# Kernel tuning notes

Measured on AMD Instinct MI355X. Metric: run time of the kernel, lower is better.

The kernel has to match this reference:

```python
import jax, jax.numpy as jnp
import numpy as np

B, NN, T, H, P = 4, 50000, 1, 64, 5   # batch, nodes/graph, time steps, hidden, prediction steps
E = 1_200_000                          # edges over the flattened batched graph
N = B * NN                             # total flattened nodes


def setup_inputs() -> dict:
    key = jax.random.key(0)
    ks = jax.random.split(key, 10)
    x = jax.random.normal(ks[0], (B, NN, T), jnp.float32)
    edge_index = jax.random.randint(ks[1], (2, E), 0, N)
    edge_weight = jax.random.uniform(ks[2], (E,), jnp.float32)
    h = jnp.zeros((B, NN, H), jnp.float32)
    s = lambda k, shp, fan: (jax.random.normal(k, shp, jnp.float32) / np.float32(np.sqrt(fan)))
    W1 = s(ks[3], (T, H), T); b1 = jnp.zeros((H,), jnp.float32)
    W2 = s(ks[4], (H, H), H); b2 = jnp.zeros((H,), jnp.float32)
    w_ih = s(ks[5], (3 * H, H), H)
    w_hh = s(ks[6], (3 * H, H), H)
    b_ih = jnp.zeros((3 * H,), jnp.float32)
    b_hh = jnp.zeros((3 * H,), jnp.float32)
    fc_w = s(ks[7], (H, P), H); fc_b = jnp.zeros((P,), jnp.float32)
    return dict(x=x, edge_weight=edge_weight, h=h, W1=W1, b1=b1, W2=W2, b2=b2,
                w_ih=w_ih, w_hh=w_hh, b_ih=b_ih, b_hh=b_hh, fc_w=fc_w, fc_b=fc_b,
                edge_index=edge_index)


def _gcn(xf, src, dst, ew, dinv, W, b):
    # PyG GCNConv: x' = D^-1/2 (A + I) D^-1/2 (x W) + b, self-loop weight 1
    xw = xf @ W                                  # [N, H]
    norm = dinv[src] * ew * dinv[dst]            # [E]
    agg = jax.ops.segment_sum(xw[src] * norm[:, None], dst, num_segments=N)
    return agg + (dinv * dinv)[:, None] * xw + b  # self-loop term + bias


def reference(x, edge_weight, h, W1, b1, W2, b2, w_ih, w_hh, b_ih, b_hh, fc_w, fc_b, edge_index):
    src, dst = edge_index[0], edge_index[1]
    # degree includes self-loop weight 1 (PyG add_self_loops fill_value=1)
    deg = jax.ops.segment_sum(edge_weight, dst, num_segments=N) + 1.0
    dinv = jax.lax.rsqrt(deg)

    xf = x.reshape(N, T)
    xf = jax.nn.relu(_gcn(xf, src, dst, edge_weight, dinv, W1, b1))
    xf = jax.nn.relu(_gcn(xf, src, dst, edge_weight, dinv, W2, b2))

    # torch GRUCell
    hf = h.reshape(N, H)
    gi = xf @ w_ih.T + b_ih
    gh = hf @ w_hh.T + b_hh
    i_r, i_z, i_n = jnp.split(gi, 3, axis=1)
    h_r, h_z, h_n = jnp.split(gh, 3, axis=1)
    r = jax.nn.sigmoid(i_r + h_r)
    z = jax.nn.sigmoid(i_z + h_z)
    n = jnp.tanh(i_n + r * h_n)
    h_new = (1.0 - z) * n + z * hf

    out = h_new @ fc_w + fc_b
    return out.reshape(B, NN, P), h_new.reshape(B, NN, H)
```

## Files before the change

### kernel.cpp

```cpp
#include <hip/hip_runtime.h>

#define NTOT 200000
#define EE   1200000

typedef unsigned int u32;
typedef unsigned long long u64;
typedef __attribute__((ext_vector_type(8))) short short8v;
typedef __attribute__((ext_vector_type(4))) float f32x4;

__device__ __forceinline__ float rcpf(float x) { return __builtin_amdgcn_rcpf(x); }
__device__ __forceinline__ float sigm(float x) { return rcpf(1.f + __expf(-x)); }
__device__ __forceinline__ float tanh_f(float x) { return 1.f - 2.f * rcpf(__expf(2.f * x) + 1.f); }
__device__ __forceinline__ u32 f2bf(float f) {
    u32 u = __float_as_uint(f);
    return (u + 0x7fffu + ((u >> 16) & 1u)) >> 16;
}
__device__ __forceinline__ float bf2f(u32 b) { return __uint_as_float(b << 16); }
__device__ __forceinline__ float bf_lo(u32 p) { return __uint_as_float(p << 16); }
__device__ __forceinline__ float bf_hi(u32 p) { return __uint_as_float(p & 0xffff0000u); }

__device__ __forceinline__ short8v packhi8(const float* v) {
    union { u32 u[4]; short8v s; } r;
    r.u[0] = f2bf(v[0]) | (f2bf(v[1]) << 16);
    r.u[1] = f2bf(v[2]) | (f2bf(v[3]) << 16);
    r.u[2] = f2bf(v[4]) | (f2bf(v[5]) << 16);
    r.u[3] = f2bf(v[6]) | (f2bf(v[7]) << 16);
    return r.s;
}
__device__ __forceinline__ short8v packlo8(const float* v) {
    float q[8];
    #pragma unroll
    for (int i = 0; i < 8; ++i) q[i] = v[i] - bf2f(f2bf(v[i]));
    union { u32 u[4]; short8v s; } r;
    r.u[0] = f2bf(q[0]) | (f2bf(q[1]) << 16);
    r.u[1] = f2bf(q[2]) | (f2bf(q[3]) << 16);
    r.u[2] = f2bf(q[4]) | (f2bf(q[5]) << 16);
    r.u[3] = f2bf(q[6]) | (f2bf(q[7]) << 16);
    return r.s;
}

__global__ __launch_bounds__(256) void k_degcnt(const float* __restrict__ ew,
                                                const int* __restrict__ dst,
                                                u64* __restrict__ pk,
                                                u32* __restrict__ rank) {
    int e = blockIdx.x*256 + threadIdx.x;
    if (e < EE) {
        u64 v = (1ull << 40) | (u64)(u32)__float2uint_rn(ew[e] * 16777216.f);
        u64 old = atomicAdd(&pk[dst[e]], v);
        rank[e] = (u32)(old >> 40);
    }
}

__global__ __launch_bounds__(256) void k_scan1(const u64* __restrict__ pk,
                                               int* __restrict__ off,
                                               int* __restrict__ bsum,
                                               float* __restrict__ dinv) {
    __shared__ int s[256];
    int t = threadIdx.x, i = blockIdx.x*256 + t;
    int v = 0;
    if (i < NTOT) {
        u64 p = pk[i];
        v = (int)(p >> 40);
        dinv[i] = rsqrtf(1.0f + (float)(p & 0xFFFFFFFFFFull) * 5.9604644775390625e-8f);
    }
    s[t] = v; __syncthreads();
    #pragma unroll
    for (int o = 1; o < 256; o <<= 1) {
        int a = (t >= o) ? s[t-o] : 0; __syncthreads();
        s[t] += a; __syncthreads();
    }
    if (i < NTOT) off[i] = s[t] - v;
    if (t == 255) bsum[blockIdx.x] = s[255];
}

__global__ __launch_bounds__(1024) void k_scan2(int* bsum) {
    __shared__ int s[1024];
    int t = threadIdx.x;
    int v = (t < 782) ? bsum[t] : 0;
    s[t] = v; __syncthreads();
    for (int o = 1; o < 1024; o <<= 1) {
        int a = (t >= o) ? s[t-o] : 0; __syncthreads();
        s[t] += a; __syncthreads();
    }
    if (t < 782) bsum[t] = s[t] - v;
}

__global__ __launch_bounds__(256) void k_scan3(int* __restrict__ off,
                                               const int* __restrict__ bsum) {
    int i = blockIdx.x*256 + threadIdx.x;
    if (i < NTOT) off[i] = off[i] + bsum[blockIdx.x];
    if (i == 0) off[NTOT] = EE;
}

__global__ __launch_bounds__(256) void k_fill(const int* __restrict__ src,
                                              const int* __restrict__ dst,
                                              const float* __restrict__ ew,
                                              const float* __restrict__ dinv,
                                              const int* __restrict__ off,
                                              const u32* __restrict__ rank,
                                              uint2* __restrict__ epack) {
    int e = blockIdx.x*256 + threadIdx.x;
    if (e >= EE) return;
    int d = dst[e], s = src[e];
    float norm = dinv[s] * ew[e] * dinv[d];
    int p = off[d] + (int)rank[e];
    epack[p] = make_uint2((u32)s, __float_as_uint(norm));
}

__global__ __launch_bounds__(256) void k_sagg(const int* __restrict__ off,
                                              const uint2* __restrict__ epack,
                                              const float* __restrict__ x,
                                              const float* __restrict__ dinv,
                                              float* __restrict__ sagg) {
    int n = blockIdx.x*256 + threadIdx.x;
    if (n >= NTOT) return;
    int e0 = off[n], e1 = off[n+1];
    float s = 0.f;
    for (int e = e0; e < e1; ++e) {
        uint2 ep = epack[e];
        s += __uint_as_float(ep.y) * x[ep.x];
    }
    float di = dinv[n];
    sagg[n] = s + di*di*x[n];
}

__global__ __launch_bounds__(256) void k_wprep(const float* __restrict__ wih,
                                               const float* __restrict__ whh,
                                               uint4* __restrict__ wpack) {
    int v = blockIdx.x*256 + threadIdx.x;
    if (v >= 3072) return;
    int lane = v & 63, tau = v >> 6;
    const float* W = (tau < 24) ? wih : whh;
    int tt = tau % 24;
    int lt = tt >> 1, ks = tt & 1;
    const float* s = W + (lt*16 + (lane & 15))*64 + ks*32 + (lane >> 4)*8;
    uint4 o;
    o.x = f2bf(s[0]) | (f2bf(s[1]) << 16);
    o.y = f2bf(s[2]) | (f2bf(s[3]) << 16);
    o.z = f2bf(s[4]) | (f2bf(s[5]) << 16);
    o.w = f2bf(s[6]) | (f2bf(s[7]) << 16);
    wpack[v] = o;
}

__global__ __launch_bounds__(256) void k_l12(const float* __restrict__ sagg,
                                             const float* __restrict__ W1,
                                             const float* __restrict__ b1,
                                             const float* __restrict__ W2,
                                             u32* __restrict__ A2p) {
    __shared__ float ysh[64][68];
    __shared__ float wsh[64*68];
    int t = threadIdx.x;
    int n0 = blockIdx.x * 64;
    #pragma unroll
    for (int i = 0; i < 16; ++i) {
        int v = t + i*256;
        wsh[(v >> 6)*68 + (v & 63)] = W2[v];
    }
    {
        int row = t >> 2, c0 = (t & 3) * 16;
        float sv = sagg[n0 + row];
        #pragma unroll
        for (int q = 0; q < 4; ++q) {
            float4 w  = *(const float4*)(W1 + c0 + q*4);
            float4 bb = *(const float4*)(b1 + c0 + q*4);
            ysh[row][c0+q*4+0] = fmaxf(sv*w.x + bb.x, 0.f);
            ysh[row][c0+q*4+1] = fmaxf(sv*w.y + bb.y, 0.f);
            ysh[row][c0+q*4+2] = fmaxf(sv*w.z + bb.z, 0.f);
            ysh[row][c0+q*4+3] = fmaxf(sv*w.w + bb.w, 0.f);
        }
    }
    __syncthreads();
    int p = t >> 3, c = t & 7;
    float acc0[8], acc1[8];
    #pragma unroll
    for (int j = 0; j < 8; ++j) { acc0[j] = 0.f; acc1[j] = 0.f; }
    #pragma unroll 4
    for (int k = 0; k < 64; ++k) {
        float y0 = ysh[p][k], y1 = ysh[p+32][k];
        const float* wr = wsh + k*68 + c*8;
        float4 w0 = *(const float4*)wr;
        float4 w1 = *(const float4*)(wr + 4);
        acc0[0] += y0*w0.x; acc0[1] += y0*w0.y; acc0[2] += y0*w0.z; acc0[3] += y0*w0.w;
        acc0[4] += y0*w1.x; acc0[5] += y0*w1.y; acc0[6] += y0*w1.z; acc0[7] += y0*w1.w;
        acc1[0] += y1*w0.x; acc1[1] += y1*w0.y; acc1[2] += y1*w0.z; acc1[3] += y1*w0.w;
        acc1[4] += y1*w1.x; acc1[5] += y1*w1.y; acc1[6] += y1*w1.z; acc1[7] += y1*w1.w;
    }
    int na = n0 + p, nb = n0 + p + 32;
    uint4 pk;
    pk.x = f2bf(acc0[0]) | (f2bf(acc0[1]) << 16);
    pk.y = f2bf(acc0[2]) | (f2bf(acc0[3]) << 16);
    pk.z = f2bf(acc0[4]) | (f2bf(acc0[5]) << 16);
    pk.w = f2bf(acc0[6]) | (f2bf(acc0[7]) << 16);
    *(uint4*)(A2p + (size_t)na*32 + c*4) = pk;
    pk.x = f2bf(acc1[0]) | (f2bf(acc1[1]) << 16);
    pk.y = f2bf(acc1[2]) | (f2bf(acc1[3]) << 16);
    pk.z = f2bf(acc1[4]) | (f2bf(acc1[5]) << 16);
    pk.w = f2bf(acc1[6]) | (f2bf(acc1[7]) << 16);
    *(uint4*)(A2p + (size_t)nb*32 + c*4) = pk;
}

__global__ __launch_bounds__(256) void k_gather(const u32* __restrict__ A2p,
                                                const uint2* __restrict__ epack,
                                                const int* __restrict__ off,
                                                const float* __restrict__ dinv,
                                                const float* __restrict__ b2,
                                                float* __restrict__ B2) {
    int wv = (blockIdx.x*256 + threadIdx.x) >> 6;
    int lane = threadIdx.x & 63;
    if (wv >= NTOT) return;
    int g = lane >> 4, q = lane & 15;
    int e0 = off[wv], e1 = off[wv+1];
    float ax = 0.f, ay = 0.f, az = 0.f, aw = 0.f;
    for (int e = e0 + g; e < e1; e += 4) {
        uint2 ep = epack[e];
        int sr = (int)ep.x;
        float nrm = __uint_as_float(ep.y);
        uint2 pw = *(const uint2*)(A2p + (size_t)sr*32 + q*2);
        ax += nrm*bf_lo(pw.x); ay += nrm*bf_hi(pw.x);
        az += nrm*bf_lo(pw.y); aw += nrm*bf_hi(pw.y);
    }
    ax += __shfl_xor(ax, 16); ax += __shfl_xor(ax, 32);
    ay += __shfl_xor(ay, 16); ay += __shfl_xor(ay, 32);
    az += __shfl_xor(az, 16); az += __shfl_xor(az, 32);
    aw += __shfl_xor(aw, 16); aw += __shfl_xor(aw, 32);
    if (g == 0) {
        float di = dinv[wv], d2 = di*di;
        uint2 pw = *(const uint2*)(A2p + (size_t)wv*32 + q*2);
        float4 bb = *(const float4*)(b2 + q*4);
        float4 o;
        o.x = fmaxf(ax + d2*bf_lo(pw.x) + bb.x, 0.f);
        o.y = fmaxf(ay + d2*bf_hi(pw.x) + bb.y, 0.f);
        o.z = fmaxf(az + d2*bf_lo(pw.y) + bb.z, 0.f);
        o.w = fmaxf(aw + d2*bf_hi(pw.y) + bb.w, 0.f);
        *(float4*)(B2 + (size_t)wv*64 + q*4) = o;
    }
}

__global__ __launch_bounds__(256) void k_gru(const float* B2,
                                             const float* __restrict__ h_in,
                                             const uint4* __restrict__ wpack,
                                             const float* __restrict__ bih,
                                             const float* __restrict__ bhh,
                                             const float* __restrict__ fcw,
                                             const float* __restrict__ fcb,
                                             float* __restrict__ out,
                                             float* hnew) {
    int t = threadIdx.x;
    int lane = t & 63, w = t >> 6;
    int n0 = blockIdx.x * 64;
    int rowA = n0 + w*16 + (lane & 15);
    int kb = (lane >> 4) * 8;
    float yf[16], hb[16];
    {
        const float4* yp = (const float4*)(B2 + (size_t)rowA*64 + kb);
        const float4* hp = (const float4*)(h_in + (size_t)rowA*64 + kb);
        *(float4*)&yf[0]  = yp[0]; *(float4*)&yf[4]  = yp[1];
        *(float4*)&yf[8]  = yp[8]; *(float4*)&yf[12] = yp[9];
        *(float4*)&hb[0]  = hp[0]; *(float4*)&hb[4]  = hp[1];
        *(float4*)&hb[8]  = hp[8]; *(float4*)&hb[12] = hp[9];
    }
    short8v ya0h = packhi8(&yf[0]), ya1h = packhi8(&yf[8]);
    short8v ya0l = packlo8(&yf[0]), ya1l = packlo8(&yf[8]);
    short8v ha0h = packhi8(&hb[0]), ha1h = packhi8(&hb[8]);
    short8v ha0l = packlo8(&hb[0]), ha1l = packlo8(&hb[8]);
    float po[4][5] = {};
    #pragma unroll
    for (int lt = 0; lt < 4; ++lt) {
        short8v wbr0 = *(const short8v*)&wpack[(lt*2+0)*64 + lane];
        short8v wbr1 = *(const short8v*)&wpack[(lt*2+1)*64 + lane];
        short8v wbz0 = *(const short8v*)&wpack[((lt+4)*2+0)*64 + lane];
        short8v wbz1 = *(const short8v*)&wpack[((lt+4)*2+1)*64 + lane];
        short8v wbn0 = *(const short8v*)&wpack[((lt+8)*2+0)*64 + lane];
        short8v wbn1 = *(const short8v*)&wpack[((lt+8)*2+1)*64 + lane];
        short8v vbr0 = *(const short8v*)&wpack[1536 + (lt*2+0)*64 + lane];
        short8v vbr1 = *(const short8v*)&wpack[1536 + (lt*2+1)*64 + lane];
        short8v vbz0 = *(const short8v*)&wpack[1536 + ((lt+4)*2+0)*64 + lane];
        short8v vbz1 = *(const short8v*)&wpack[1536 + ((lt+4)*2+1)*64 + lane];
        short8v vbn0 = *(const short8v*)&wpack[1536 + ((lt+8)*2+0)*64 + lane];
        short8v vbn1 = *(const short8v*)&wpack[1536 + ((lt+8)*2+1)*64 + lane];
        f32x4 aR  = {0.f,0.f,0.f,0.f};
        f32x4 aZ  = {0.f,0.f,0.f,0.f};
        f32x4 aNi = {0.f,0.f,0.f,0.f};
        f32x4 aNh = {0.f,0.f,0.f,0.f};
        aR = __builtin_amdgcn_mfma_f32_16x16x32_bf16(ya0h, wbr0, aR, 0, 0, 0);
        aR = __builtin_amdgcn_mfma_f32_16x16x32_bf16(ya1h, wbr1, aR, 0, 0, 0);
        aR = __builtin_amdgcn_mfma_f32_16x16x32_bf16(ya0l, wbr0, aR, 0, 0, 0);
        aR = __builtin_amdgcn_mfma_f32_16x16x32_bf16(ya1l, wbr1, aR, 0, 0, 0);
        aR = __builtin_amdgcn_mfma_f32_16x16x32_bf16(ha0h, vbr0, aR, 0, 0, 0);
        aR = __builtin_amdgcn_mfma_f32_16x16x32_bf16(ha1h, vbr1, aR, 0, 0, 0);
        aR = __builtin_amdgcn_mfma_f32_16x16x32_bf16(ha0l, vbr0, aR, 0, 0, 0);
        aR = __builtin_amdgcn_mfma_f32_16x16x32_bf16(ha1l, vbr1, aR, 0, 0, 0);
        aZ = __builtin_amdgcn_mfma_f32_16x16x32_bf16(ya0h, wbz0, aZ, 0, 0, 0);
        aZ = __builtin_amdgcn_mfma_f32_16x16x32_bf16(ya1h, wbz1, aZ, 0, 0, 0);
        aZ = __builtin_amdgcn_mfma_f32_16x16x32_bf16(ya0l, wbz0, aZ, 0, 0, 0);
        aZ = __builtin_amdgcn_mfma_f32_16x16x32_bf16(ya1l, wbz1, aZ, 0, 0, 0);
        aZ = __builtin_amdgcn_mfma_f32_16x16x32_bf16(ha0h, vbz0, aZ, 0, 0, 0);
        aZ = __builtin_amdgcn_mfma_f32_16x16x32_bf16(ha1h, vbz1, aZ, 0, 0, 0);
        aZ = __builtin_amdgcn_mfma_f32_16x16x32_bf16(ha0l, vbz0, aZ, 0, 0, 0);
        aZ = __builtin_amdgcn_mfma_f32_16x16x32_bf16(ha1l, vbz1, aZ, 0, 0, 0);
        aNi = __builtin_amdgcn_mfma_f32_16x16x32_bf16(ya0h, wbn0, aNi, 0, 0, 0);
        aNi = __builtin_amdgcn_mfma_f32_16x16x32_bf16(ya1h, wbn1, aNi, 0, 0, 0);
        aNi = __builtin_amdgcn_mfma_f32_16x16x32_bf16(ya0l, wbn0, aNi, 0, 0, 0);
        aNi = __builtin_amdgcn_mfma_f32_16x16x32_bf16(ya1l, wbn1, aNi, 0, 0, 0);
        aNh = __builtin_amdgcn_mfma_f32_16x16x32_bf16(ha0h, vbn0, aNh, 0, 0, 0);
        aNh = __builtin_amdgcn_mfma_f32_16x16x32_bf16(ha1h, vbn1, aNh, 0, 0, 0);
        aNh = __builtin_amdgcn_mfma_f32_16x16x32_bf16(ha0l, vbn0, aNh, 0, 0, 0);
        aNh = __builtin_amdgcn_mfma_f32_16x16x32_bf16(ha1l, vbn1, aNh, 0, 0, 0);
        int l = lt*16 + (lane & 15);
        float br = bih[l] + bhh[l];
        float bz = bih[64+l] + bhh[64+l];
        float bn = bih[128+l];
        float cn = bhh[128+l];
        float fw0 = fcw[l*5+0], fw1 = fcw[l*5+1], fw2 = fcw[l*5+2],
              fw3 = fcw[l*5+3], fw4 = fcw[l*5+4];
        #pragma unroll
        for (int r4 = 0; r4 < 4; ++r4) {
            int row = n0 + w*16 + (lane >> 4)*4 + r4;
            float rg = sigm(aR[r4] + br);
            float zg = sigm(aZ[r4] + bz);
            float ng = tanh_f(aNi[r4] + bn + rg*(aNh[r4] + cn));
            float hfv = h_in[(size_t)row*64 + l];
            float hnv = (1.f - zg)*ng + zg*hfv;
            hnew[(size_t)row*64 + l] = hnv;
            po[r4][0] += hnv*fw0; po[r4][1] += hnv*fw1; po[r4][2] += hnv*fw2;
            po[r4][3] += hnv*fw3; po[r4][4] += hnv*fw4;
        }
    }
    #pragma unroll
    for (int r4 = 0; r4 < 4; ++r4)
        #pragma unroll
        for (int j = 0; j < 5; ++j) {
            float v = po[r4][j];
            v += __shfl_xor(v, 1); v += __shfl_xor(v, 2);
            v += __shfl_xor(v, 4); v += __shfl_xor(v, 8);
            po[r4][j] = v;
        }
    if ((lane & 15) == 0) {
        #pragma unroll
        for (int r4 = 0; r4 < 4; ++r4) {
            int node = n0 + w*16 + (lane >> 4)*4 + r4;
            #pragma unroll
            for (int j = 0; j < 5; ++j) out[(size_t)node*5 + j] = po[r4][j] + fcb[j];
        }
    }
}

extern "C" void kernel_launch(void* const* d_in, const int* in_sizes, int n_in,
                              void* d_out, int out_size, void* d_ws, size_t ws_size,
                              hipStream_t stream) {
    const float* x   = (const float*)d_in[0];
    const float* ew  = (const float*)d_in[1];
    const float* h   = (const float*)d_in[2];
    const float* W1  = (const float*)d_in[3];
    const float* b1  = (const float*)d_in[4];
    const float* W2  = (const float*)d_in[5];
    const float* b2  = (const float*)d_in[6];
    const float* wih = (const float*)d_in[7];
    const float* whh = (const float*)d_in[8];
    const float* bih = (const float*)d_in[9];
    const float* bhh = (const float*)d_in[10];
    const float* fcw = (const float*)d_in[11];
    const float* fcb = (const float*)d_in[12];
    const int*   ei  = (const int*)d_in[13];
    const int* src = ei;
    const int* dst = ei + EE;

    u32*   A2p   = (u32*)d_ws;
    uint2* epack = (uint2*)((char*)d_ws + 25600000);
    uint4* wpack = (uint4*)((char*)d_ws + 35200000);
    u64*   pk    = (u64*)((char*)d_ws + 36000000);
    u32*   rank  = (u32*)((char*)d_ws + 38000000);
    int*   off  = (int*)d_out;
    int*   bsum = off + NTOT + 1;
    float* dinv = (float*)d_out + 401024;
    float* sagg = (float*)d_out + 601024;
    float* out  = (float*)d_out;
    float* B2   = out + (size_t)NTOT*5;

    hipMemsetAsync(pk, 0, (size_t)NTOT*8, stream);
    k_degcnt<<<4688,  256, 0, stream>>>(ew, dst, pk, rank);
    k_scan1 <<<782,   256, 0, stream>>>(pk, off, bsum, dinv);
    k_scan2 <<<1,    1024, 0, stream>>>(bsum);
    k_scan3 <<<782,   256, 0, stream>>>(off, bsum);
    k_fill  <<<4688,  256, 0, stream>>>(src, dst, ew, dinv, off, rank, epack);
    k_sagg  <<<782,   256, 0, stream>>>(off, epack, x, dinv, sagg);
    k_wprep <<<12,    256, 0, stream>>>(wih, whh, wpack);
    k_l12   <<<3125,  256, 0, stream>>>(sagg, W1, b1, W2, A2p);
    k_gather<<<50000, 256, 0, stream>>>(A2p, epack, off, dinv, b2, B2);
    k_gru   <<<3125,  256, 0, stream>>>(B2, h, wpack, bih, bhh, fcw, fcb, out, B2);
}
```

Baseline: 279.5 us.

## Fuse layer-2 edge gather into GRU kernel via shared-memory staging

Merges the per-node gather kernel (second GCN aggregation) into the GRU/MFMA kernel. Each wave gathers 16 nodes sequentially into shared memory, and h is staged in shared memory too, so the fp32 B2 intermediate never goes to and from global memory and one launch is removed. In exchange, each wave walks its 16 nodes serially, which cuts memory-level parallelism for the latency-bound gather. Scratch arrays are also moved from the output buffer into the workspace.

```diff
diff --git a/kernel.cpp b/kernel.cpp
--- a/kernel.cpp
+++ b/kernel.cpp
@@ -199,66 +199,70 @@
     *(uint4*)(A2p + (size_t)nb*32 + c*4) = pk;
 }
 
-__global__ __launch_bounds__(256) void k_gather(const u32* __restrict__ A2p,
-                                                const uint2* __restrict__ epack,
-                                                const int* __restrict__ off,
-                                                const float* __restrict__ dinv,
-                                                const float* __restrict__ b2,
-                                                float* __restrict__ B2) {
-    int wv = (blockIdx.x*256 + threadIdx.x) >> 6;
-    int lane = threadIdx.x & 63;
-    if (wv >= NTOT) return;
-    int g = lane >> 4, q = lane & 15;
-    int e0 = off[wv], e1 = off[wv+1];
-    float ax = 0.f, ay = 0.f, az = 0.f, aw = 0.f;
-    for (int e = e0 + g; e < e1; e += 4) {
-        uint2 ep = epack[e];
-        int sr = (int)ep.x;
-        float nrm = __uint_as_float(ep.y);
-        uint2 pw = *(const uint2*)(A2p + (size_t)sr*32 + q*2);
-        ax += nrm*bf_lo(pw.x); ay += nrm*bf_hi(pw.x);
-        az += nrm*bf_lo(pw.y); aw += nrm*bf_hi(pw.y);
-    }
-    ax += __shfl_xor(ax, 16); ax += __shfl_xor(ax, 32);
-    ay += __shfl_xor(ay, 16); ay += __shfl_xor(ay, 32);
-    az += __shfl_xor(az, 16); az += __shfl_xor(az, 32);
-    aw += __shfl_xor(aw, 16); aw += __shfl_xor(aw, 32);
-    if (g == 0) {
-        float di = dinv[wv], d2 = di*di;
-        uint2 pw = *(const uint2*)(A2p + (size_t)wv*32 + q*2);
-        float4 bb = *(const float4*)(b2 + q*4);
-        float4 o;
-        o.x = fmaxf(ax + d2*bf_lo(pw.x) + bb.x, 0.f);
-        o.y = fmaxf(ay + d2*bf_hi(pw.x) + bb.y, 0.f);
-        o.z = fmaxf(az + d2*bf_lo(pw.y) + bb.z, 0.f);
-        o.w = fmaxf(aw + d2*bf_hi(pw.y) + bb.w, 0.f);
-        *(float4*)(B2 + (size_t)wv*64 + q*4) = o;
-    }
-}
-
-__global__ __launch_bounds__(256) void k_gru(const float* B2,
-                                             const float* __restrict__ h_in,
-                                             const uint4* __restrict__ wpack,
-                                             const float* __restrict__ bih,
-                                             const float* __restrict__ bhh,
-                                             const float* __restrict__ fcw,
-                                             const float* __restrict__ fcb,
-                                             float* __restrict__ out,
-                                             float* hnew) {
+__global__ __launch_bounds__(256) void k_ggru(const u32* __restrict__ A2p,
+                                              const uint2* __restrict__ epack,
+                                              const int* __restrict__ off,
+                                              const float* __restrict__ dinv,
+                                              const float* __restrict__ b2,
+                                              const float* __restrict__ h_in,
+                                              const uint4* __restrict__ wpack,
+                                              const float* __restrict__ bih,
+                                              const float* __restrict__ bhh,
+                                              const float* __restrict__ fcw,
+                                              const float* __restrict__ fcb,
+                                              float* __restrict__ out,
+                                              float* __restrict__ hnew) {
+    __shared__ float ysh[64][68];
+    __shared__ float hsh[64][68];
     int t = threadIdx.x;
     int lane = t & 63, w = t >> 6;
     int n0 = blockIdx.x * 64;
-    int rowA = n0 + w*16 + (lane & 15);
+    {
+        int r = t >> 2, qq = t & 3;
+        const float4* hp = (const float4*)(h_in + (size_t)(n0 + r)*64 + qq*16);
+        float4* dp = (float4*)&hsh[r][qq*16];
+        dp[0] = hp[0]; dp[1] = hp[1]; dp[2] = hp[2]; dp[3] = hp[3];
+    }
+    int g = lane >> 4, q = lane & 15;
+    for (int i = 0; i < 16; ++i) {
+        int node = n0 + w*16 + i;
+        int e0 = off[node], e1 = off[node+1];
+        float ax = 0.f, ay = 0.f, az = 0.f, av = 0.f;
+        for (int e = e0 + g; e < e1; e += 4) {
+            uint2 ep = epack[e];
+            float nrm = __uint_as_float(ep.y);
+            uint2 pw = *(const uint2*)(A2p + (size_t)ep.x*32 + q*2);
+            ax += nrm*bf_lo(pw.x); ay += nrm*bf_hi(pw.x);
+            az += nrm*bf_lo(pw.y); av += nrm*bf_hi(pw.y);
+        }
+        ax += __shfl_xor(ax, 16); ax += __shfl_xor(ax, 32);
+        ay += __shfl_xor(ay, 16); ay += __shfl_xor(ay, 32);
+        az += __shfl_xor(az, 16); az += __shfl_xor(az, 32);
+        av += __shfl_xor(av, 16); av += __shfl_xor(av, 32);
+        if (g == 0) {
+            float di = dinv[node], d2 = di*di;
+            uint2 pw = *(const uint2*)(A2p + (size_t)node*32 + q*2);
+            float4 bb = *(const float4*)(b2 + q*4);
+            float4 o;
+            o.x = fmaxf(ax + d2*bf_lo(pw.x) + bb.x, 0.f);
+            o.y = fmaxf(ay + d2*bf_hi(pw.x) + bb.y, 0.f);
+            o.z = fmaxf(az + d2*bf_lo(pw.y) + bb.z, 0.f);
+            o.w = fmaxf(av + d2*bf_hi(pw.y) + bb.w, 0.f);
+            *(float4*)&ysh[w*16 + i][q*4] = o;
+        }
+    }
+    __syncthreads();
+    int rowL = w*16 + (lane & 15);
     int kb = (lane >> 4) * 8;
     float yf[16], hb[16];
-    {
-        const float4* yp = (const float4*)(B2 + (size_t)rowA*64 + kb);
-        const float4* hp = (const float4*)(h_in + (size_t)rowA*64 + kb);
-        *(float4*)&yf[0]  = yp[0]; *(float4*)&yf[4]  = yp[1];
-        *(float4*)&yf[8]  = yp[8]; *(float4*)&yf[12] = yp[9];
-        *(float4*)&hb[0]  = hp[0]; *(float4*)&hb[4]  = hp[1];
-        *(float4*)&hb[8]  = hp[8]; *(float4*)&hb[12] = hp[9];
-    }
+    *(float4*)&yf[0]  = *(const float4*)&ysh[rowL][kb];
+    *(float4*)&yf[4]  = *(const float4*)&ysh[rowL][kb+4];
+    *(float4*)&yf[8]  = *(const float4*)&ysh[rowL][kb+32];
+    *(float4*)&yf[12] = *(const float4*)&ysh[rowL][kb+36];
+    *(float4*)&hb[0]  = *(const float4*)&hsh[rowL][kb];
+    *(float4*)&hb[4]  = *(const float4*)&hsh[rowL][kb+4];
+    *(float4*)&hb[8]  = *(const float4*)&hsh[rowL][kb+32];
+    *(float4*)&hb[12] = *(const float4*)&hsh[rowL][kb+36];
     short8v ya0h = packhi8(&yf[0]), ya1h = packhi8(&yf[8]);
     short8v ya0l = packlo8(&yf[0]), ya1l = packlo8(&yf[8]);
     short8v ha0h = packhi8(&hb[0]), ha1h = packhi8(&hb[8]);
@@ -315,13 +319,13 @@
               fw3 = fcw[l*5+3], fw4 = fcw[l*5+4];
         #pragma unroll
         for (int r4 = 0; r4 < 4; ++r4) {
-            int row = n0 + w*16 + (lane >> 4)*4 + r4;
+            int rl = w*16 + (lane >> 4)*4 + r4;
             float rg = sigm(aR[r4] + br);
             float zg = sigm(aZ[r4] + bz);
             float ng = tanh_f(aNi[r4] + bn + rg*(aNh[r4] + cn));
-            float hfv = h_in[(size_t)row*64 + l];
+            float hfv = hsh[rl][l];
             float hnv = (1.f - zg)*ng + zg*hfv;
-            hnew[(size_t)row*64 + l] = hnv;
+            hnew[(size_t)(n0 + rl)*64 + l] = hnv;
             po[r4][0] += hnv*fw0; po[r4][1] += hnv*fw1; po[r4][2] += hnv*fw2;
             po[r4][3] += hnv*fw3; po[r4][4] += hnv*fw4;
         }
@@ -370,22 +374,22 @@
     uint4* wpack = (uint4*)((char*)d_ws + 35200000);
     u64*   pk    = (u64*)((char*)d_ws + 36000000);
     u32*   rank  = (u32*)((char*)d_ws + 38000000);
-    int*   off  = (int*)d_out;
-    int*   bsum = off + NTOT + 1;
-    float* dinv = (float*)d_out + 401024;
-    float* sagg = (float*)d_out + 601024;
+    int*   off   = (int*)((char*)d_ws + 43000000);
+    int*   bsum  = (int*)((char*)d_ws + 44000000);
+    float* dinv  = (float*)((char*)d_ws + 45000000);
+    float* sagg  = (float*)((char*)d_ws + 46000000);
     float* out  = (float*)d_out;
-    float* B2   = out + (size_t)NTOT*5;
+    float* hnew = out + (size_t)NTOT*5;
 
     hipMemsetAsync(pk, 0, (size_t)NTOT*8, stream);
-    k_degcnt<<<4688,  256, 0, stream>>>(ew, dst, pk, rank);
-    k_scan1 <<<782,   256, 0, stream>>>(pk, off, bsum, dinv);
-    k_scan2 <<<1,    1024, 0, stream>>>(bsum);
-    k_scan3 <<<782,   256, 0, stream>>>(off, bsum);
-    k_fill  <<<4688,  256, 0, stream>>>(src, dst, ew, dinv, off, rank, epack);
-    k_sagg  <<<782,   256, 0, stream>>>(off, epack, x, dinv, sagg);
-    k_wprep <<<12,    256, 0, stream>>>(wih, whh, wpack);
-    k_l12   <<<3125,  256, 0, stream>>>(sagg, W1, b1, W2, A2p);
-    k_gather<<<50000, 256, 0, stream>>>(A2p, epack, off, dinv, b2, B2);
-    k_gru   <<<3125,  256, 0, stream>>>(B2, h, wpack, bih, bhh, fcw, fcb, out, B2);
-}
+    k_degcnt<<<4688, 256, 0, stream>>>(ew, dst, pk, rank);
+    k_scan1 <<<782,  256, 0, stream>>>(pk, off, bsum, dinv);
+    k_scan2 <<<1,   1024, 0, stream>>>(bsum);
+    k_scan3 <<<782,  256, 0, stream>>>(off, bsum);
+    k_fill  <<<4688, 256, 0, stream>>>(src, dst, ew, dinv, off, rank, epack);
+    k_sagg  <<<782,  256, 0, stream>>>(off, epack, x, dinv, sagg);
+    k_wprep <<<12,   256, 0, stream>>>(wih, whh, wpack);
+    k_l12   <<<3125, 256, 0, stream>>>(sagg, W1, b1, W2, A2p);
+    k_ggru  <<<3125, 256, 0, stream>>>(A2p, epack, off, dinv, b2, h, wpack,
+                                       bih, bhh, fcw, fcb, out, hnew);
+}
```

Result: slower. 386.7 us (+38.3%).
